# Performance work log

Measured on AMD Instinct MI355X. Metric: run time of the kernel, lower is better.

Reference implementation:

```python
import jax, jax.numpy as jnp
import numpy as np

EMB_DIM = 512
HEAD_DIM = 512


def setup_inputs() -> dict:
    key = jax.random.key(0)
    ks = jax.random.split(key, 7)
    B, S = 4, 2048
    lim = 1.0 / np.sqrt(EMB_DIM)  # torch Linear default init range
    x = jax.random.normal(ks[0], (B, S, EMB_DIM), dtype=jnp.float32)
    Wq = jax.random.uniform(ks[1], (HEAD_DIM, EMB_DIM), jnp.float32, -lim, lim)
    Wk = jax.random.uniform(ks[2], (HEAD_DIM, EMB_DIM), jnp.float32, -lim, lim)
    Wv = jax.random.uniform(ks[3], (HEAD_DIM, EMB_DIM), jnp.float32, -lim, lim)
    bq = jax.random.uniform(ks[4], (HEAD_DIM,), jnp.float32, -lim, lim)
    bk = jax.random.uniform(ks[5], (HEAD_DIM,), jnp.float32, -lim, lim)
    bv = jax.random.uniform(ks[6], (HEAD_DIM,), jnp.float32, -lim, lim)
    return {"x": x, "Wq": Wq, "bq": bq, "Wk": Wk, "bk": bk, "Wv": Wv, "bv": bv}


def reference(x, Wq, bq, Wk, bk, Wv, bv):
    # torch nn.Linear: y = x @ W.T + b
    q = jnp.einsum('bse,de->bsd', x, Wq) + bq
    k = jnp.einsum('bse,de->bsd', x, Wk) + bk
    v = jnp.einsum('bse,de->bsd', x, Wv) + bv
    scale = jnp.sqrt(jnp.asarray(HEAD_DIM, dtype=q.dtype))
    scores = jnp.einsum('bqd,bkd->bqk', q, k) / scale  # [B,S,S]
    S = x.shape[1]
    causal = jnp.triu(jnp.ones((S, S), dtype=bool), k=1)  # True above diagonal
    scores = jnp.where(causal[None, :, :], -jnp.inf, scores)
    attn = jax.nn.softmax(scores, axis=-1)
    return jnp.einsum('bqk,bkd->bqd', attn, v)
```

## Files before the change

kernel.cpp:

```cpp
#include <hip/hip_runtime.h>
#include <hip/hip_bf16.h>
#include <cstdint>
#include <math.h>

#define S_LEN 2048
#define D_DIM 512
#define NROWS 8192
#define NQKV  1536
#define QK_SCALE 0.04419417382415922f

typedef unsigned short u16;
typedef unsigned long long u64;
typedef __attribute__((ext_vector_type(8))) short short8;
typedef __attribute__((ext_vector_type(4))) float floatx4;

__device__ inline floatx4 mfma16(short8 a, short8 b, floatx4 c){
  return __builtin_amdgcn_mfma_f32_16x16x32_bf16(a, b, c, 0, 0, 0);
}
__device__ inline u16 f2b(float f){
  uint32_t u = __float_as_uint(f);
  u = (u + 0x7fffu + ((u >> 16) & 1u)) >> 16;
  return (u16)u;
}
__device__ inline float b2f(u16 u){ return __uint_as_float(((uint32_t)u) << 16); }
#define GLD16(g, l) __builtin_amdgcn_global_load_lds( \
    (const __attribute__((address_space(1))) void*)(g), \
    (__attribute__((address_space(3))) void*)(l), 16, 0, 0)

__global__ void cvt_kernel(const float* __restrict__ x,
                           const float* __restrict__ Wq,
                           const float* __restrict__ Wk,
                           const float* __restrict__ Wv,
                           u16* __restrict__ xw)
{
  const int NT4 = (NROWS * D_DIM) / 4 + (NQKV * D_DIM) / 4;
  for (int i = blockIdx.x * blockDim.x + threadIdx.x; i < NT4;
       i += gridDim.x * blockDim.x) {
    int e = i * 4;
    const float* src;
    if (e < NROWS * D_DIM) {
      src = x + e;
    } else {
      int j = e - NROWS * D_DIM;
      if (j < 512 * 512)           src = Wq + j;
      else if (j < 2 * 512 * 512)  src = Wk + (j - 512 * 512);
      else                         src = Wv + (j - 2 * 512 * 512);
    }
    float4 v = *(const float4*)src;
    ushort4 o;
    o.x = f2b(v.x); o.y = f2b(v.y); o.z = f2b(v.z); o.w = f2b(v.w);
    *(ushort4*)(xw + e) = o;
  }
}

__launch_bounds__(256)
__global__ void qkv_gemm(const u16* __restrict__ xb,
                         const u16* __restrict__ wb,
                         const float* __restrict__ bq,
                         const float* __restrict__ bk,
                         const float* __restrict__ bv,
                         u16* __restrict__ qb,
                         u16* __restrict__ kb,
                         u16* __restrict__ vt)
{
  __shared__ alignas(16) u16 sm[2][16384];
  const int tid = threadIdx.x;
  const int l = tid & 63, w = tid >> 6;
  const int lr = l & 15, lg = l >> 4;
  const int wr = w >> 1, wc = w & 1;
  const int bid = blockIdx.x;
  const int xcd = bid & 7;
  const int t = bid >> 3;
  const int bn = t % 12, bmhi = t / 12;
  const int bm = (bmhi << 3) | xcd;
  const int m0 = bm * 128, n0 = bn * 128;

  const u16* gA = xb + (size_t)(m0 + (tid >> 3)) * D_DIM + (tid & 7) * 8;
  const u16* gB = wb + (size_t)(n0 + (tid >> 3)) * D_DIM + (tid & 7) * 8;

#define STAGEK(BUF, KT) { \
  char* la = (char*)&sm[BUF][0] + tid * 16; \
  char* lb = (char*)&sm[BUF][8192] + tid * 16; \
  const u16* ga = gA + (KT) * 64; \
  const u16* gb = gB + (KT) * 64; \
  _Pragma("unroll") for (int jj = 0; jj < 4; jj++) { \
    GLD16(ga + (size_t)jj * 32 * D_DIM, la + jj * 4096); \
    GLD16(gb + (size_t)jj * 32 * D_DIM, lb + jj * 4096); } }

  floatx4 acc[4][4];
#pragma unroll
  for (int m = 0; m < 4; m++)
#pragma unroll
    for (int n = 0; n < 4; n++) acc[m][n] = 0.0f;

  STAGEK(0, 0)
  __syncthreads();

  for (int kt = 0; kt < 8; ++kt) {
    const int cb = kt & 1;
    if (kt < 7) STAGEK(cb ^ 1, kt + 1)
#pragma unroll
    for (int kk = 0; kk < 2; ++kk) {
      short8 a[4], bfr[4];
#pragma unroll
      for (int m = 0; m < 4; m++)
        a[m] = *(const short8*)&sm[cb][(wr * 64 + m * 16 + lr) * 64 + kk * 32 + lg * 8];
#pragma unroll
      for (int n = 0; n < 4; n++)
        bfr[n] = *(const short8*)&sm[cb][8192 + (wc * 64 + n * 16 + lr) * 64 + kk * 32 + lg * 8];
#pragma unroll
      for (int m = 0; m < 4; m++)
#pragma unroll
        for (int n = 0; n < 4; n++)
          acc[m][n] = mfma16(a[m], bfr[n], acc[m][n]);
    }
    __syncthreads();
  }
#undef STAGEK

  if (n0 < 1024) {
    const float* bias = (n0 < 512) ? bq : bk;
    u16* dst = (n0 < 512) ? qb : kb;
    const float scl = (n0 < 512) ? QK_SCALE : 1.0f;
    const int nbase = n0 & 511;
#pragma unroll
    for (int n = 0; n < 4; n++) {
      int gn = nbase + wc * 64 + n * 16 + lr;
      float bia = bias[gn];
#pragma unroll
      for (int m = 0; m < 4; m++) {
        int gm0 = m0 + wr * 64 + m * 16 + lg * 4;
#pragma unroll
        for (int r = 0; r < 4; r++)
          dst[(size_t)(gm0 + r) * D_DIM + gn] = f2b((acc[m][n][r] + bia) * scl);
      }
    }
  } else {
    const int nbase = n0 - 1024;
    const int bIdx = m0 >> 11;
    const int s0 = m0 & 2047;
    __syncthreads();
#pragma unroll
    for (int h = 0; h < 2; ++h) {
      if (wc == h) {
#pragma unroll
        for (int n = 0; n < 4; n++) {
          int lrow = n * 16 + lr;
          float bia = bv[nbase + h * 64 + lrow];
#pragma unroll
          for (int m = 0; m < 4; m++) {
            int lcol = wr * 64 + m * 16 + lg * 4;
#pragma unroll
            for (int r = 0; r < 4; r++)
              sm[0][lrow * 136 + lcol + r] = f2b(acc[m][n][r] + bia);
          }
        }
      }
      __syncthreads();
      {
        int row = tid >> 2;
        int c0 = (tid & 3) * 32;
        u16* dstp = vt + (size_t)bIdx * D_DIM * S_LEN
                       + (size_t)(nbase + h * 64 + row) * S_LEN + s0 + c0;
        const u16* srcp = &sm[0][row * 136 + c0];
#pragma unroll
        for (int jj = 0; jj < 4; jj++)
          *(short8*)(dstp + jj * 8) = *(const short8*)(srcp + jj * 8);
      }
      __syncthreads();
    }
  }
}

__launch_bounds__(256)
__global__ void s_gemm(const u16* __restrict__ qb,
                       const u16* __restrict__ kb,
                       u16* __restrict__ P,
                       float* __restrict__ pRS)
{
  __shared__ alignas(16) u16 sm[2][16384];
  const int tid = threadIdx.x;
  const int l = tid & 63, w = tid >> 6;
  const int lr = l & 15, lg = l >> 4;
  const int wr = w >> 1, wc = w & 1;
  const int bid = blockIdx.x;
  const int xcd = bid & 7;
  const int b = xcd >> 1;
  const int j = (bid >> 3) * 2 + (xcd & 1);
  float g = sqrtf(8.f * (float)j + 1.f);
  int qt = (int)((g - 1.f) * 0.5f + 1e-4f);
  while ((qt + 1) * (qt + 2) / 2 <= j) ++qt;
  while (qt * (qt + 1) / 2 > j) --qt;
  const int kt = j - qt * (qt + 1) / 2;

  const u16* gA = kb + ((size_t)(b * S_LEN + kt * 128 + (tid >> 3))) * D_DIM + (tid & 7) * 8;
  const u16* gB = qb + ((size_t)(b * S_LEN + qt * 128 + (tid >> 3))) * D_DIM + (tid & 7) * 8;

#define STAGES(BUF, KT) { \
  char* la = (char*)&sm[BUF][0] + tid * 16; \
  char* lb = (char*)&sm[BUF][8192] + tid * 16; \
  const u16* ga = gA + (KT) * 64; \
  const u16* gb = gB + (KT) * 64; \
  _Pragma("unroll") for (int jj = 0; jj < 4; jj++) { \
    GLD16(ga + (size_t)jj * 32 * D_DIM, la + jj * 4096); \
    GLD16(gb + (size_t)jj * 32 * D_DIM, lb + jj * 4096); } }

  floatx4 acc[4][4];
#pragma unroll
  for (int m = 0; m < 4; m++)
#pragma unroll
    for (int n = 0; n < 4; n++) acc[m][n] = 0.0f;

  STAGES(0, 0)
  __syncthreads();
  for (int ks = 0; ks < 8; ++ks) {
    const int cb = ks & 1;
    if (ks < 7) STAGES(cb ^ 1, ks + 1)
#pragma unroll
    for (int kk = 0; kk < 2; ++kk) {
      short8 a[4], bfr[4];
#pragma unroll
      for (int m = 0; m < 4; m++)
        a[m] = *(const short8*)&sm[cb][(wr * 64 + m * 16 + lr) * 64 + kk * 32 + lg * 8];
#pragma unroll
      for (int n = 0; n < 4; n++)
        bfr[n] = *(const short8*)&sm[cb][8192 + (wc * 64 + n * 16 + lr) * 64 + kk * 32 + lg * 8];
#pragma unroll
      for (int m = 0; m < 4; m++)
#pragma unroll
        for (int n = 0; n < 4; n++)
          acc[m][n] = mfma16(a[m], bfr[n], acc[m][n]);
    }
    __syncthreads();
  }
#undef STAGES

  const bool diag = (kt == qt);
  u16* Pb = P + (size_t)b * S_LEN * S_LEN;
#pragma unroll
  for (int n = 0; n < 4; ++n) {
    const int q = qt * 128 + wc * 64 + n * 16 + lr;
    float rs = 0.f;
#pragma unroll
    for (int m = 0; m < 4; ++m) {
      const int kb0 = kt * 128 + wr * 64 + m * 16 + lg * 4;
      u16 h[4];
#pragma unroll
      for (int r = 0; r < 4; ++r) {
        float e = __expf(acc[m][n][r]);
        if (diag && (kb0 + r > q)) e = 0.f;
        h[r] = f2b(e);
        rs += b2f(h[r]);
      }
      u64 pk = (u64)h[0] | ((u64)h[1] << 16) | ((u64)h[2] << 32) | ((u64)h[3] << 48);
      *(u64*)(Pb + (size_t)q * S_LEN + kb0) = pk;
    }
    rs += __shfl_xor(rs, 16);
    rs += __shfl_xor(rs, 32);
    if (lg == 0)
      pRS[(size_t)(b * S_LEN + q) * 32 + kt * 2 + wr] = rs;
  }
}

__launch_bounds__(256)
__global__ void pv_gemm(const u16* __restrict__ P,
                       const float* __restrict__ pRS,
                       const u16* __restrict__ vt,
                       float* __restrict__ out)
{
  __shared__ alignas(16) u16 sm[2][12288];
  __shared__ float rinv[64];

  const int tid = threadIdx.x;
  const int l = tid & 63, w = tid >> 6;
  const int lr = l & 15, lg = l >> 4;
  const int wr = w >> 1, wc = w & 1;
  const int bid = blockIdx.x;
  const int xcd = bid & 7;
  const int b = xcd >> 1, xl = xcd & 1;
  const int t = bid >> 3;
  const int m = t & 3;
  const int qraw = ((t >> 2) << 1) | xl;
  const int qt = 31 - qraw;
  const int m0 = m * 128;
  const int q0 = qt * 64;
  const int nks = qt + 1;

  const u16* gA = vt + (size_t)b * D_DIM * S_LEN
                     + (size_t)(m0 + (tid >> 3)) * S_LEN + (tid & 7) * 8;
  const u16* gB = P + (size_t)b * S_LEN * S_LEN
                    + (size_t)(q0 + (tid >> 3)) * S_LEN + (tid & 7) * 8;

  {
    const int qi = tid >> 2;
    const int qrow = q0 + qi;
    const int ns = ((qrow >> 7) + 1) * 2;
    float s = 0.f;
    for (int ss = tid & 3; ss < ns; ss += 4)
      s += pRS[(size_t)(b * S_LEN + qrow) * 32 + ss];
    s += __shfl_xor(s, 1);
    s += __shfl_xor(s, 2);
    if ((tid & 3) == 0) rinv[qi] = 1.0f / s;
  }

#define STAGEPV(BUF, KS) { \
  char* la = (char*)&sm[BUF][0] + tid * 16; \
  char* lb = (char*)&sm[BUF][8192] + tid * 16; \
  const u16* ga = gA + (KS) * 64; \
  const u16* gb = gB + (KS) * 64; \
  _Pragma("unroll") for (int jj = 0; jj < 4; jj++) \
    GLD16(ga + (size_t)jj * 32 * S_LEN, la + jj * 4096); \
  _Pragma("unroll") for (int jj = 0; jj < 2; jj++) \
    GLD16(gb + (size_t)jj * 32 * S_LEN, lb + jj * 4096); }

  floatx4 acc[4][2];
#pragma unroll
  for (int mm = 0; mm < 4; mm++) { acc[mm][0] = 0.0f; acc[mm][1] = 0.0f; }

  STAGEPV(0, 0)
  __syncthreads();
  for (int ks = 0; ks < nks; ++ks) {
    const int cb = ks & 1;
    if (ks < nks - 1) STAGEPV(cb ^ 1, ks + 1)
#pragma unroll
    for (int kk = 0; kk < 2; ++kk) {
      short8 a[4], bfr[2];
#pragma unroll
      for (int mm = 0; mm < 4; mm++)
        a[mm] = *(const short8*)&sm[cb][(wr * 64 + mm * 16 + lr) * 64 + kk * 32 + lg * 8];
#pragma unroll
      for (int n = 0; n < 2; n++)
        bfr[n] = *(const short8*)&sm[cb][8192 + (wc * 32 + n * 16 + lr) * 64 + kk * 32 + lg * 8];
#pragma unroll
      for (int mm = 0; mm < 4; mm++)
#pragma unroll
        for (int n = 0; n < 2; n++)
          acc[mm][n] = mfma16(a[mm], bfr[n], acc[mm][n]);
    }
    __syncthreads();
  }
#undef STAGEPV

#pragma unroll
  for (int n = 0; n < 2; ++n) {
    const int q = q0 + wc * 32 + n * 16 + lr;
    const float inv = rinv[wc * 32 + n * 16 + lr];
    float* op = out + (size_t)(b * S_LEN + q) * D_DIM + m0 + wr * 64 + lg * 4;
#pragma unroll
    for (int mm = 0; mm < 4; ++mm) {
      float4 v;
      v.x = acc[mm][n][0] * inv;
      v.y = acc[mm][n][1] * inv;
      v.z = acc[mm][n][2] * inv;
      v.w = acc[mm][n][3] * inv;
      *(float4*)(op + mm * 16) = v;
    }
  }
}

extern "C" void kernel_launch(void* const* d_in, const int* in_sizes, int n_in,
                              void* d_out, int out_size, void* d_ws, size_t ws_size,
                              hipStream_t stream)
{
  const float* x  = (const float*)d_in[0];
  const float* Wq = (const float*)d_in[1];
  const float* bq = (const float*)d_in[2];
  const float* Wk = (const float*)d_in[3];
  const float* bk = (const float*)d_in[4];
  const float* Wv = (const float*)d_in[5];
  const float* bv = (const float*)d_in[6];
  float* out = (float*)d_out;

  u16* xw = (u16*)d_ws;
  u16* xb = xw;
  u16* wb = xb + (size_t)NROWS * D_DIM;
  u16* qb = wb + (size_t)NQKV * D_DIM;
  u16* kb = qb + (size_t)NROWS * D_DIM;
  u16* vt = kb + (size_t)NROWS * D_DIM;
  u16* P  = vt + (size_t)NROWS * D_DIM;
  float* pRS = (float*)(P + (size_t)4 * S_LEN * S_LEN);

  hipLaunchKernelGGL(cvt_kernel, dim3(2048), dim3(256), 0, stream, x, Wq, Wk, Wv, xw);
  hipLaunchKernelGGL(qkv_gemm, dim3(768), dim3(256), 0, stream,
                     xb, wb, bq, bk, bv, qb, kb, vt);
  hipLaunchKernelGGL(s_gemm, dim3(544), dim3(256), 0, stream, qb, kb, P, pRS);
  hipLaunchKernelGGL(pv_gemm, dim3(512), dim3(256), 0, stream, P, pRS, vt, out);
}
```

Baseline: 92.93 us.

## Replace double-buffered LDS staging with single buffer and widen PV k-step

```diff
diff --git a/kernel.cpp b/kernel.cpp
--- a/kernel.cpp
+++ b/kernel.cpp
@@ -63,7 +63,7 @@
                          u16* __restrict__ kb,
                          u16* __restrict__ vt)
 {
-  __shared__ alignas(16) u16 sm[2][16384];
+  __shared__ alignas(16) u16 sm[16384];
   const int tid = threadIdx.x;
   const int l = tid & 63, w = tid >> 6;
   const int lr = l & 15, lg = l >> 4;
@@ -78,9 +78,9 @@
   const u16* gA = xb + (size_t)(m0 + (tid >> 3)) * D_DIM + (tid & 7) * 8;
   const u16* gB = wb + (size_t)(n0 + (tid >> 3)) * D_DIM + (tid & 7) * 8;
 
-#define STAGEK(BUF, KT) { \
-  char* la = (char*)&sm[BUF][0] + tid * 16; \
-  char* lb = (char*)&sm[BUF][8192] + tid * 16; \
+#define STAGEK(KT) { \
+  char* la = (char*)&sm[0] + tid * 16; \
+  char* lb = (char*)&sm[8192] + tid * 16; \
   const u16* ga = gA + (KT) * 64; \
   const u16* gb = gB + (KT) * 64; \
   _Pragma("unroll") for (int jj = 0; jj < 4; jj++) { \
@@ -93,21 +93,18 @@
 #pragma unroll
     for (int n = 0; n < 4; n++) acc[m][n] = 0.0f;
 
-  STAGEK(0, 0)
-  __syncthreads();
-
   for (int kt = 0; kt < 8; ++kt) {
-    const int cb = kt & 1;
-    if (kt < 7) STAGEK(cb ^ 1, kt + 1)
+    STAGEK(kt)
+    __syncthreads();
 #pragma unroll
     for (int kk = 0; kk < 2; ++kk) {
       short8 a[4], bfr[4];
 #pragma unroll
       for (int m = 0; m < 4; m++)
-        a[m] = *(const short8*)&sm[cb][(wr * 64 + m * 16 + lr) * 64 + kk * 32 + lg * 8];
+        a[m] = *(const short8*)&sm[(wr * 64 + m * 16 + lr) * 64 + kk * 32 + lg * 8];
 #pragma unroll
       for (int n = 0; n < 4; n++)
-        bfr[n] = *(const short8*)&sm[cb][8192 + (wc * 64 + n * 16 + lr) * 64 + kk * 32 + lg * 8];
+        bfr[n] = *(const short8*)&sm[8192 + (wc * 64 + n * 16 + lr) * 64 + kk * 32 + lg * 8];
 #pragma unroll
       for (int m = 0; m < 4; m++)
 #pragma unroll
@@ -139,7 +136,6 @@
     const int nbase = n0 - 1024;
     const int bIdx = m0 >> 11;
     const int s0 = m0 & 2047;
-    __syncthreads();
 #pragma unroll
     for (int h = 0; h < 2; ++h) {
       if (wc == h) {
@@ -152,7 +148,7 @@
             int lcol = wr * 64 + m * 16 + lg * 4;
 #pragma unroll
             for (int r = 0; r < 4; r++)
-              sm[0][lrow * 136 + lcol + r] = f2b(acc[m][n][r] + bia);
+              sm[lrow * 136 + lcol + r] = f2b(acc[m][n][r] + bia);
           }
         }
       }
@@ -162,7 +158,7 @@
         int c0 = (tid & 3) * 32;
         u16* dstp = vt + (size_t)bIdx * D_DIM * S_LEN
                        + (size_t)(nbase + h * 64 + row) * S_LEN + s0 + c0;
-        const u16* srcp = &sm[0][row * 136 + c0];
+        const u16* srcp = &sm[row * 136 + c0];
 #pragma unroll
         for (int jj = 0; jj < 4; jj++)
           *(short8*)(dstp + jj * 8) = *(const short8*)(srcp + jj * 8);
@@ -178,7 +174,7 @@
                        u16* __restrict__ P,
                        float* __restrict__ pRS)
 {
-  __shared__ alignas(16) u16 sm[2][16384];
+  __shared__ alignas(16) u16 sm[16384];
   const int tid = threadIdx.x;
   const int l = tid & 63, w = tid >> 6;
   const int lr = l & 15, lg = l >> 4;
@@ -196,9 +192,9 @@
   const u16* gA = kb + ((size_t)(b * S_LEN + kt * 128 + (tid >> 3))) * D_DIM + (tid & 7) * 8;
   const u16* gB = qb + ((size_t)(b * S_LEN + qt * 128 + (tid >> 3))) * D_DIM + (tid & 7) * 8;
 
-#define STAGES(BUF, KT) { \
-  char* la = (char*)&sm[BUF][0] + tid * 16; \
-  char* lb = (char*)&sm[BUF][8192] + tid * 16; \
+#define STAGES(KT) { \
+  char* la = (char*)&sm[0] + tid * 16; \
+  char* lb = (char*)&sm[8192] + tid * 16; \
   const u16* ga = gA + (KT) * 64; \
   const u16* gb = gB + (KT) * 64; \
   _Pragma("unroll") for (int jj = 0; jj < 4; jj++) { \
@@ -211,20 +207,18 @@
 #pragma unroll
     for (int n = 0; n < 4; n++) acc[m][n] = 0.0f;
 
-  STAGES(0, 0)
-  __syncthreads();
   for (int ks = 0; ks < 8; ++ks) {
-    const int cb = ks & 1;
-    if (ks < 7) STAGES(cb ^ 1, ks + 1)
+    STAGES(ks)
+    __syncthreads();
 #pragma unroll
     for (int kk = 0; kk < 2; ++kk) {
       short8 a[4], bfr[4];
 #pragma unroll
       for (int m = 0; m < 4; m++)
-        a[m] = *(const short8*)&sm[cb][(wr * 64 + m * 16 + lr) * 64 + kk * 32 + lg * 8];
+        a[m] = *(const short8*)&sm[(wr * 64 + m * 16 + lr) * 64 + kk * 32 + lg * 8];
 #pragma unroll
       for (int n = 0; n < 4; n++)
-        bfr[n] = *(const short8*)&sm[cb][8192 + (wc * 64 + n * 16 + lr) * 64 + kk * 32 + lg * 8];
+        bfr[n] = *(const short8*)&sm[8192 + (wc * 64 + n * 16 + lr) * 64 + kk * 32 + lg * 8];
 #pragma unroll
       for (int m = 0; m < 4; m++)
 #pragma unroll
@@ -268,7 +262,7 @@
                        const u16* __restrict__ vt,
                        float* __restrict__ out)
 {
-  __shared__ alignas(16) u16 sm[2][12288];
+  __shared__ alignas(16) u16 sm[24576];
   __shared__ float rinv[64];
 
   const int tid = threadIdx.x;
@@ -284,12 +278,10 @@
   const int qt = 31 - qraw;
   const int m0 = m * 128;
   const int q0 = qt * 64;
-  const int nks = qt + 1;
-
-  const u16* gA = vt + (size_t)b * D_DIM * S_LEN
-                     + (size_t)(m0 + (tid >> 3)) * S_LEN + (tid & 7) * 8;
-  const u16* gB = P + (size_t)b * S_LEN * S_LEN
-                    + (size_t)(q0 + (tid >> 3)) * S_LEN + (tid & 7) * 8;
+  const int nks = (qt >> 1) + 1;
+
+  const u16* gAb = vt + (size_t)b * D_DIM * S_LEN + (size_t)m0 * S_LEN;
+  const u16* gBb = P + (size_t)b * S_LEN * S_LEN + (size_t)q0 * S_LEN;
 
   {
     const int qi = tid >> 2;
@@ -303,34 +295,34 @@
     if ((tid & 3) == 0) rinv[qi] = 1.0f / s;
   }
 
-#define STAGEPV(BUF, KS) { \
-  char* la = (char*)&sm[BUF][0] + tid * 16; \
-  char* lb = (char*)&sm[BUF][8192] + tid * 16; \
-  const u16* ga = gA + (KS) * 64; \
-  const u16* gb = gB + (KS) * 64; \
-  _Pragma("unroll") for (int jj = 0; jj < 4; jj++) \
-    GLD16(ga + (size_t)jj * 32 * S_LEN, la + jj * 4096); \
-  _Pragma("unroll") for (int jj = 0; jj < 2; jj++) \
-    GLD16(gb + (size_t)jj * 32 * S_LEN, lb + jj * 4096); }
-
   floatx4 acc[4][2];
 #pragma unroll
   for (int mm = 0; mm < 4; mm++) { acc[mm][0] = 0.0f; acc[mm][1] = 0.0f; }
 
-  STAGEPV(0, 0)
-  __syncthreads();
   for (int ks = 0; ks < nks; ++ks) {
-    const int cb = ks & 1;
-    if (ks < nks - 1) STAGEPV(cb ^ 1, ks + 1)
-#pragma unroll
-    for (int kk = 0; kk < 2; ++kk) {
+    const int kv0 = ks * 128;
+#pragma unroll
+    for (int i = 0; i < 8; ++i) {
+      const int bo = tid * 16 + i * 4096;
+      const int row = bo >> 8, colb = bo & 255;
+      GLD16(gAb + (size_t)row * S_LEN + kv0 + (colb >> 1), (char*)&sm[0] + bo);
+    }
+#pragma unroll
+    for (int i = 0; i < 4; ++i) {
+      const int bo = tid * 16 + i * 4096;
+      const int row = bo >> 8, colb = bo & 255;
+      GLD16(gBb + (size_t)row * S_LEN + kv0 + (colb >> 1), (char*)&sm[16384] + bo);
+    }
+    __syncthreads();
+#pragma unroll
+    for (int kk = 0; kk < 4; ++kk) {
       short8 a[4], bfr[2];
 #pragma unroll
       for (int mm = 0; mm < 4; mm++)
-        a[mm] = *(const short8*)&sm[cb][(wr * 64 + mm * 16 + lr) * 64 + kk * 32 + lg * 8];
+        a[mm] = *(const short8*)&sm[(wr * 64 + mm * 16 + lr) * 128 + kk * 32 + lg * 8];
 #pragma unroll
       for (int n = 0; n < 2; n++)
-        bfr[n] = *(const short8*)&sm[cb][8192 + (wc * 32 + n * 16 + lr) * 64 + kk * 32 + lg * 8];
+        bfr[n] = *(const short8*)&sm[16384 + (wc * 32 + n * 16 + lr) * 128 + kk * 32 + lg * 8];
 #pragma unroll
       for (int mm = 0; mm < 4; mm++)
 #pragma unroll
@@ -339,7 +331,6 @@
     }
     __syncthreads();
   }
-#undef STAGEPV
 
 #pragma unroll
   for (int n = 0; n < 2; ++n) {
```

New measurement: 114.4 us. 23.1% more time.
